# Performance work log

Measured on AMD Instinct MI355X. Metric: run time of the kernel, lower is better.

## Reference

```python
import jax, jax.numpy as jnp
import numpy as np

B, T, EMB, NDIM = 8, 2048, 1024, 1024


def setup_inputs() -> dict:
    key = jax.random.key(0)
    k1, k2, k3, k4 = jax.random.split(key, 4)
    X = jax.random.normal(k1, (B, T, EMB), dtype=jnp.float32)
    # Linear(emb, ndim, bias=False); stored as [emb, ndim] so projection is X @ W.
    scale = 1.0 / np.sqrt(EMB)
    Wq = jax.random.normal(k2, (EMB, NDIM), dtype=jnp.float32) * scale
    Wk = jax.random.normal(k3, (EMB, NDIM), dtype=jnp.float32) * scale
    Wv = jax.random.normal(k4, (EMB, NDIM), dtype=jnp.float32) * scale
    return {"X": X, "Wq": Wq, "Wk": Wk, "Wv": Wv}


def reference(X, Wq, Wk, Wv):
    ndim = Wq.shape[-1]
    T_ = X.shape[1]
    Q = X @ Wq  # [B,T,ndim]
    K = X @ Wk  # [B,T,ndim]
    V = X @ Wv  # [B,T,ndim]
    # scores[b,t,s] = Q[b,t] . K[b,s], scaled by ndim^-0.5
    scores = jnp.einsum("btd,bsd->bts", Q, K) * (ndim ** -0.5)
    mask = jnp.tril(jnp.ones((T_, T_), dtype=bool))  # causal lower-triangular
    scores = jnp.where(mask, scores, -jnp.inf)
    # NOTE: source uses F.softmax(..., dim=1) -> normalize over the QUERY axis
    # (columns of the [T,T] matrix), not the usual key axis. Replicated faithfully.
    probs = jax.nn.softmax(scores, axis=1)
    # dropout is identity in eval / p=0 deterministic baseline
    return probs @ V  # [B,T,ndim]
```

## Files before the change

kernel.cpp:

```cpp
#include <hip/hip_runtime.h>
#include <hip/hip_bf16.h>

#define B_   8
#define T_   2048
#define EMB_ 1024
#define ND_  1024
#define NTB2 8

typedef __attribute__((ext_vector_type(8))) short   bf8_t;
typedef __attribute__((ext_vector_type(4))) float   f32x4;

__device__ __forceinline__ unsigned short f2bf(float f) {
  union { float f; unsigned int u; } c; c.f = f;
  unsigned int u = c.u;
  unsigned int r = (u + 0x7FFFu + ((u >> 16) & 1u)) >> 16;
  return (unsigned short)r;
}

__device__ __forceinline__ float bf2f(unsigned short b) {
  union { unsigned int u; float f; } c; c.u = ((unsigned int)b) << 16;
  return c.f;
}

__device__ __forceinline__ void gload_lds16(const unsigned short* g, unsigned short* l) {
  __builtin_amdgcn_global_load_lds(
      (const __attribute__((address_space(1))) unsigned int*)g,
      (__attribute__((address_space(3))) unsigned int*)l,
      16, 0, 0);
}

#define SB0() __builtin_amdgcn_sched_barrier(0)
#define BAR() __builtin_amdgcn_s_barrier()

__device__ __forceinline__ void stage_half(const unsigned short* __restrict__ g, int lda,
                                           unsigned short* lhalf, int wave, int lane) {
  const int r3 = lane >> 3, c3 = lane & 7;
  const int colsw = ((c3 ^ r3) << 3);
#pragma unroll
  for (int j = 0; j < 2; ++j) {
    const int row = wave * 8 + r3 + 64 * j;
    gload_lds16(g + (size_t)row * lda + colsw, lhalf + wave * 512 + j * 4096);
  }
}

__device__ __forceinline__ bf8_t read_frag(const unsigned short* half, int r, int ks, int lane) {
  const int col = (((ks) << 5) + ((lane >> 4) << 3)) ^ ((r & 7) << 3);
  return *(const bf8_t*)(half + r * 64 + col);
}

__device__ __forceinline__ int swz_ep(int x) { return ((x >> 1) & 7) << 4; }

__global__ void __launch_bounds__(256) cvt_x_kernel(const float* __restrict__ in,
                                                    unsigned short* __restrict__ out) {
  const int i = (blockIdx.x * 256 + threadIdx.x) * 4;
  float4 v = *(const float4*)(in + i);
  ushort4 o = make_ushort4(f2bf(v.x), f2bf(v.y), f2bf(v.z), f2bf(v.w));
  *(ushort4*)(out + i) = o;
}

__global__ void __launch_bounds__(256) transpose_w3_kernel(const float* __restrict__ Wq,
                                                           const float* __restrict__ Wk,
                                                           const float* __restrict__ Wv,
                                                           unsigned short* __restrict__ Wt3) {
  __shared__ unsigned short tile[32][33];
  const int z = blockIdx.z;
  const float* W = (z == 0) ? Wq : (z == 1) ? Wk : Wv;
  const float cscale = (z == 0) ? 0.03125f : 1.0f;
  unsigned short* Wt = Wt3 + (size_t)z * ND_ * EMB_;
  const int n0 = blockIdx.x * 32, k0 = blockIdx.y * 32;
  const int tx = threadIdx.x & 31, ty = threadIdx.x >> 5;
#pragma unroll
  for (int r = 0; r < 32; r += 8) {
    float v = W[(size_t)(k0 + ty + r) * ND_ + n0 + tx];
    tile[tx][ty + r] = f2bf(v * cscale);
  }
  __syncthreads();
#pragma unroll
  for (int r = 0; r < 32; r += 8) {
    Wt[(size_t)(n0 + ty + r) * EMB_ + k0 + tx] = tile[ty + r][tx];
  }
}

#define MFMA_QUAD(MB, AF, AOFF) do { \
  __builtin_amdgcn_s_setprio(1); \
  _Pragma("unroll") \
  for (int mi = 0; mi < 2; ++mi) \
    _Pragma("unroll") \
    for (int nf = 0; nf < 4; ++nf) \
      _Pragma("unroll") \
      for (int ks = 0; ks < 2; ++ks) \
        acc[(MB) * 2 + mi][nf] = __builtin_amdgcn_mfma_f32_16x16x32_bf16( \
            (AF)[(AOFF) + mi][ks], bfr[nf][ks], acc[(MB) * 2 + mi][nf], 0, 0, 0); \
  __builtin_amdgcn_s_setprio(0); \
} while (0)

#define MFMA_Q8(MB) do { \
  __builtin_amdgcn_s_setprio(1); \
  _Pragma("unroll") \
  for (int nf = 0; nf < 4; ++nf) \
    _Pragma("unroll") \
    for (int ks = 0; ks < 2; ++ks) \
      acc[(MB)][nf] = __builtin_amdgcn_mfma_f32_16x16x32_bf16( \
          af[(MB)][ks], bfr[nf][ks], acc[(MB)][nf], 0, 0, 0); \
  __builtin_amdgcn_s_setprio(0); \
} while (0)

#define LDSA(d, h) (lds256 + ((d) * 2 + (h)) * 8192)
#define LDSB(d, h) (lds256 + 32768 + ((d) * 2 + (h)) * 8192)

#define GEMM256_LOOP(ABASE, BBASE, LDK) \
  stage_half((ABASE),                             (LDK), LDSA(0, 0), wave, lane); \
  stage_half((ABASE) + (size_t)128 * (LDK),       (LDK), LDSA(0, 1), wave, lane); \
  stage_half((BBASE),                             (LDK), LDSB(0, 0), wave, lane); \
  stage_half((BBASE) + (size_t)128 * (LDK),       (LDK), LDSB(0, 1), wave, lane); \
  stage_half((BBASE) + 64,                        (LDK), LDSB(1, 0), wave, lane); \
  stage_half((BBASE) + (size_t)128 * (LDK) + 64,  (LDK), LDSB(1, 1), wave, lane); \
  stage_half((ABASE) + 64,                        (LDK), LDSA(1, 0), wave, lane); \
  stage_half((ABASE) + (size_t)128 * (LDK) + 64,  (LDK), LDSA(1, 1), wave, lane); \
  asm volatile("s_waitcnt vmcnt(8)" ::: "memory"); \
  SB0(); BAR(); SB0(); \
  for (int t = 0; t < 16; ++t) { \
    const int d = t & 1; \
    const unsigned short* Ah = LDSA(d, wm); \
    const unsigned short* Bh = LDSB(d, wn >> 1); \
    bf8_t bfr[4][2], af[4][2]; \
    _Pragma("unroll") \
    for (int nf = 0; nf < 4; ++nf) \
      _Pragma("unroll") \
      for (int ks = 0; ks < 2; ++ks) bfr[nf][ks] = read_frag(Bh, brow + nf * 16, ks, lane); \
    _Pragma("unroll") \
    for (int mf = 0; mf < 4; ++mf) \
      _Pragma("unroll") \
      for (int ks = 0; ks < 2; ++ks) af[mf][ks] = read_frag(Ah, arow + mf * 16, ks, lane); \
    SB0(); BAR(); SB0(); \
    MFMA_QUAD(0, af, 0); \
    SB0(); \
    asm volatile("s_waitcnt lgkmcnt(0)" ::: "memory"); \
    SB0(); BAR(); SB0(); \
    if (t < 14) { \
      stage_half((BBASE) + (size_t)(t + 2) * 64,                     (LDK), LDSB(d, 0), wave, lane); \
      stage_half((BBASE) + (size_t)128 * (LDK) + (size_t)(t + 2) * 64,(LDK), LDSB(d, 1), wave, lane); \
    } \
    SB0(); BAR(); SB0(); \
    MFMA_QUAD(1, af, 2); \
    SB0(); BAR(); SB0(); \
    bf8_t af2[4][2]; \
    _Pragma("unroll") \
    for (int mf = 0; mf < 4; ++mf) \
      _Pragma("unroll") \
      for (int ks = 0; ks < 2; ++ks) af2[mf][ks] = read_frag(Ah, arow + (mf + 4) * 16, ks, lane); \
    SB0(); BAR(); SB0(); \
    MFMA_QUAD(2, af2, 0); \
    SB0(); \
    asm volatile("s_waitcnt lgkmcnt(0)" ::: "memory"); \
    SB0(); BAR(); SB0(); \
    if (t < 14) { \
      stage_half((ABASE) + (size_t)(t + 2) * 64,                     (LDK), LDSA(d, 0), wave, lane); \
      stage_half((ABASE) + (size_t)128 * (LDK) + (size_t)(t + 2) * 64,(LDK), LDSA(d, 1), wave, lane); \
      asm volatile("s_waitcnt vmcnt(8)" ::: "memory"); \
    } else if (t == 14) { \
      asm volatile("s_waitcnt vmcnt(0)" ::: "memory"); \
    } \
    SB0(); BAR(); SB0(); \
    MFMA_QUAD(3, af2, 2); \
    SB0(); BAR(); SB0(); \
  }

template <int OUTMODE>
__global__ void __launch_bounds__(512, 2)
gemm_xw256_kernel(const unsigned short* __restrict__ A,
                  const unsigned short* __restrict__ Bt,
                  unsigned short* __restrict__ C) {
  extern __shared__ unsigned short lds256[];
  const int tid = threadIdx.x, lane = tid & 63, wave = tid >> 6;
  const int wm = wave >> 2, wn = wave & 3;
  const int m0 = blockIdx.y * 256, n0 = blockIdx.x * 256;
  const unsigned short* Ab = A + (size_t)m0 * EMB_;
  const unsigned short* Bb = Bt + (size_t)n0 * EMB_;
  f32x4 acc[8][4];
#pragma unroll
  for (int i = 0; i < 8; ++i)
#pragma unroll
    for (int j = 0; j < 4; ++j)
#pragma unroll
      for (int q = 0; q < 4; ++q) acc[i][j][q] = 0.f;
  const int arow = lane & 15;
  const int brow = (wn & 1) * 64 + (lane & 15);

  GEMM256_LOOP(Ab, Bb, EMB_)

  const int cc = lane & 15, cr4 = (lane >> 4) << 2;
#pragma unroll
  for (int mf = 0; mf < 8; ++mf)
#pragma unroll
    for (int nf = 0; nf < 4; ++nf)
#pragma unroll
      for (int q = 0; q < 4; ++q) {
        const int r = wm * 128 + mf * 16 + cr4 + q;
        const int c = wn * 64 + nf * 16 + cc;
        const unsigned short bv = f2bf(acc[mf][nf][q]);
        const int byte = (OUTMODE == 1) ? (c * 512 + ((r * 2) ^ swz_ep(c)))
                                        : (r * 512 + ((c * 2) ^ swz_ep(r)));
        lds256[byte >> 1] = bv;
      }
  __syncthreads();
  if (OUTMODE == 0) {
#pragma unroll
    for (int p = 0; p < 16; ++p) {
      const int o = p * 8192 + tid * 16;
      const int ri = o >> 9, cb = o & 511;
      const bf8_t v = *(const bf8_t*)(lds256 + (((o & ~511) | (cb ^ swz_ep(ri))) >> 1));
      *(bf8_t*)(C + (size_t)(m0 + ri) * ND_ + n0 + (cb >> 1)) = v;
    }
  } else {
    const int bb = m0 >> 11, tt0 = m0 & 2047;
#pragma unroll
    for (int p = 0; p < 16; ++p) {
      const int o = p * 8192 + tid * 16;
      const int ci = o >> 9, rb = o & 511;
      const bf8_t v = *(const bf8_t*)(lds256 + (((o & ~511) | (rb ^ swz_ep(ci))) >> 1));
      *(bf8_t*)(C + ((size_t)bb * ND_ + n0 + ci) * T_ + tt0 + (rb >> 1)) = v;
    }
  }
}

__global__ void __launch_bounds__(512, 2)
scoretile576_kernel(const unsigned short* __restrict__ Qb,
                    const unsigned short* __restrict__ Kb,
                    unsigned short* __restrict__ Pp,
                    float* __restrict__ pm) {
  extern __shared__ unsigned short lds256[];
  const int id = blockIdx.x;
  const int b = id & 7;
  const int r = id >> 3;
  int sc = 0, pfx = 0;
#pragma unroll 8
  for (int i = 0; i < 8; ++i) {
    const int cnt = 16 - 2 * sc;
    if (pfx + cnt <= r) { pfx += cnt; ++sc; }
  }
  const int tr = 2 * sc + (r - pfx);
  const int t0 = tr * 128, s0 = sc * 256;
  const int tid = threadIdx.x, lane = tid & 63, wave = tid >> 6;
  const int wm = wave >> 2, wn = wave & 3;
  const int arow = lane & 15;
  const unsigned short* Ab = Qb + ((size_t)b * T_ + t0) * ND_;
  const unsigned short* Bb = Kb + ((size_t)b * T_ + s0) * ND_;
  f32x4 acc[4][4];
#pragma unroll
  for (int i = 0; i < 4; ++i)
#pragma unroll
    for (int j = 0; j < 4; ++j)
#pragma unroll
      for (int q = 0; q < 4; ++q) acc[i][j][q] = 0.f;

  stage_half(Ab,                           ND_, lds256,                     wave, lane);
  stage_half(Bb,                           ND_, lds256 + 16384,             wave, lane);
  stage_half(Bb + (size_t)128 * ND_,       ND_, lds256 + 16384 + 8192,      wave, lane);
  stage_half(Ab + 64,                      ND_, lds256 + 8192,              wave, lane);
  stage_half(Bb + 64,                      ND_, lds256 + 16384 + 2 * 8192,  wave, lane);
  stage_half(Bb + (size_t)128 * ND_ + 64,  ND_, lds256 + 16384 + 3 * 8192,  wave, lane);
  asm volatile("s_waitcnt vmcnt(6)" ::: "memory");
  SB0(); BAR(); SB0();

  for (int t = 0; t < 16; ++t) {
    const int d = t & 1;
    const unsigned short* Ah = lds256 + d * 8192;
    const unsigned short* Bh = lds256 + 16384 + (d * 2 + (wn >> 1)) * 8192;
    bf8_t bfr[4][2], af[4][2];
#pragma unroll
    for (int nf = 0; nf < 4; ++nf)
#pragma unroll
      for (int ks = 0; ks < 2; ++ks)
        bfr[nf][ks] = read_frag(Bh, (wn & 1) * 64 + nf * 16 + arow, ks, lane);
#pragma unroll
    for (int mf = 0; mf < 4; ++mf)
#pragma unroll
      for (int ks = 0; ks < 2; ++ks)
        af[mf][ks] = read_frag(Ah, wm * 64 + mf * 16 + arow, ks, lane);
    SB0(); BAR(); SB0();
    MFMA_Q8(0);
    SB0();
    asm volatile("s_waitcnt lgkmcnt(0)" ::: "memory");
    SB0(); BAR(); SB0();
    if (t < 14) {
      stage_half(Ab + (size_t)(t + 2) * 64, ND_, lds256 + d * 8192, wave, lane);
      stage_half(Bb + (size_t)(t + 2) * 64, ND_, lds256 + 16384 + (d * 2) * 8192, wave, lane);
    }
    SB0(); BAR(); SB0();
    MFMA_Q8(1);
    SB0(); BAR(); SB0();
    if (t < 14)
      stage_half(Bb + (size_t)128 * ND_ + (size_t)(t + 2) * 64, ND_, lds256 + 16384 + (d * 2 + 1) * 8192, wave, lane);
    SB0(); BAR(); SB0();
    MFMA_Q8(2);
    SB0(); BAR(); SB0();
    if (t < 14)      { asm volatile("s_waitcnt vmcnt(6)" ::: "memory"); }
    else if (t == 14){ asm volatile("s_waitcnt vmcnt(0)" ::: "memory"); }
    SB0(); BAR(); SB0();
    MFMA_Q8(3);
    SB0(); BAR(); SB0();
  }

  __syncthreads();
  const int cc = lane & 15, cr4 = (lane >> 4) << 2;
  float csum[4];
#pragma unroll
  for (int nf = 0; nf < 4; ++nf) csum[nf] = 0.f;
#pragma unroll
  for (int mf = 0; mf < 4; ++mf)
#pragma unroll
    for (int nf = 0; nf < 4; ++nf)
#pragma unroll
      for (int q = 0; q < 4; ++q) {
        const int rr = wm * 64 + mf * 16 + cr4 + q;
        const int c  = wn * 64 + nf * 16 + cc;
        const bool ok = (t0 + rr) >= (s0 + c);
        unsigned short bv = 0;
        if (ok) {
          bv = f2bf(__expf(fminf(acc[mf][nf][q], 30.f)));
          csum[nf] += bf2f(bv);
        }
        lds256[(rr * 512 + ((c * 2) ^ swz_ep(rr))) >> 1] = bv;
      }
  __syncthreads();
  unsigned short* Pbase = Pp + (size_t)b * T_ * T_;
#pragma unroll
  for (int p = 0; p < 8; ++p) {
    const int o = p * 8192 + tid * 16;
    const int ri = o >> 9, cb = o & 511;
    const bf8_t v = *(const bf8_t*)(lds256 + (((o & ~511) | (cb ^ swz_ep(ri))) >> 1));
    *(bf8_t*)(Pbase + (size_t)(t0 + ri) * T_ + s0 + (cb >> 1)) = v;
  }
#pragma unroll
  for (int nf = 0; nf < 4; ++nf) {
    csum[nf] += __shfl_xor(csum[nf], 16);
    csum[nf] += __shfl_xor(csum[nf], 32);
  }
  __syncthreads();
  float* red = (float*)lds256;
  if (lane < 16) {
#pragma unroll
    for (int nf = 0; nf < 4; ++nf)
      red[((wm * 4 + wn) * 4 + nf) * 16 + lane] = csum[nf];
  }
  __syncthreads();
  if (wm == 0 && lane < 16) {
    const size_t base = (((size_t)b * 8 + sc) * 16 + tr) * 256;
#pragma unroll
    for (int nf = 0; nf < 4; ++nf) {
      const float s = red[((0 * 4 + wn) * 4 + nf) * 16 + lane] +
                      red[((1 * 4 + wn) * 4 + nf) * 16 + lane];
      pm[base + wn * 64 + nf * 16 + lane] = s;
    }
  }
}

__global__ void __launch_bounds__(256) colreduce_kernel(const float* __restrict__ pm,
                                                        float* __restrict__ colinv) {
  const int sc = blockIdx.x, b = blockIdx.y, c = threadIdx.x;
  float l = 0.f;
  for (int tr = 2 * sc; tr < 16; ++tr)
    l += pm[(((size_t)b * 8 + sc) * 16 + tr) * 256 + c];
  colinv[(size_t)b * T_ + sc * 256 + c] = 1.0f / l;
}

__global__ void __launch_bounds__(256) vscale_kernel(unsigned short* __restrict__ Vt,
                                                     const float* __restrict__ colinv) {
  const int idx = blockIdx.x * 256 + threadIdx.x;
  const int s8 = (idx * 8) & (T_ - 1);
  const int bd = idx / (T_ / 8);
  const int b = bd >> 10;
  unsigned short* p = Vt + (size_t)bd * T_ + s8;
  bf8_t v = *(bf8_t*)p;
#pragma unroll
  for (int j = 0; j < 8; ++j) {
    const float f = bf2f((unsigned short)v[j]) * colinv[(size_t)b * T_ + s8 + j];
    v[j] = (short)f2bf(f);
  }
  *(bf8_t*)p = v;
}

__device__ __forceinline__ void pv_segment(const unsigned short* __restrict__ Ab,
                                           const unsigned short* __restrict__ Bb,
                                           float* __restrict__ Cb,
                                           int ktiles, unsigned short* lds256,
                                           int lane, int wave) {
  const int wm = wave >> 2, wn = wave & 3;
  const int arow = lane & 15;
  f32x4 acc[4][4];
#pragma unroll
  for (int i = 0; i < 4; ++i)
#pragma unroll
    for (int j = 0; j < 4; ++j)
#pragma unroll
      for (int q = 0; q < 4; ++q) acc[i][j][q] = 0.f;

  stage_half(Ab,                           T_, lds256,                     wave, lane);
  stage_half(Bb,                           T_, lds256 + 16384,             wave, lane);
  stage_half(Bb + (size_t)128 * T_,        T_, lds256 + 16384 + 8192,      wave, lane);
  stage_half(Ab + 64,                      T_, lds256 + 8192,              wave, lane);
  stage_half(Bb + 64,                      T_, lds256 + 16384 + 2 * 8192,  wave, lane);
  stage_half(Bb + (size_t)128 * T_ + 64,   T_, lds256 + 16384 + 3 * 8192,  wave, lane);
  asm volatile("s_waitcnt vmcnt(6)" ::: "memory");
  SB0(); BAR(); SB0();

  for (int t = 0; t < ktiles; ++t) {
    const int d = t & 1;
    const unsigned short* Ah = lds256 + d * 8192;
    const unsigned short* Bh = lds256 + 16384 + (d * 2 + (wn >> 1)) * 8192;
    bf8_t bfr[4][2], af[4][2];
#pragma unroll
    for (int nf = 0; nf < 4; ++nf)
#pragma unroll
      for (int ks = 0; ks < 2; ++ks)
        bfr[nf][ks] = read_frag(Bh, (wn & 1) * 64 + nf * 16 + arow, ks, lane);
#pragma unroll
    for (int mf = 0; mf < 4; ++mf)
#pragma unroll
      for (int ks = 0; ks < 2; ++ks)
        af[mf][ks] = read_frag(Ah, wm * 64 + mf * 16 + arow, ks, lane);
    SB0(); BAR(); SB0();
    MFMA_Q8(0);
    SB0();
    asm volatile("s_waitcnt lgkmcnt(0)" ::: "memory");
    SB0(); BAR(); SB0();
    if (t < ktiles - 2) {
      stage_half(Ab + (size_t)(t + 2) * 64, T_, lds256 + d * 8192, wave, lane);
      stage_half(Bb + (size_t)(t + 2) * 64, T_, lds256 + 16384 + (d * 2) * 8192, wave, lane);
    }
    SB0(); BAR(); SB0();
    MFMA_Q8(1);
    SB0(); BAR(); SB0();
    if (t < ktiles - 2)
      stage_half(Bb + (size_t)128 * T_ + (size_t)(t + 2) * 64, T_, lds256 + 16384 + (d * 2 + 1) * 8192, wave, lane);
    SB0(); BAR(); SB0();
    MFMA_Q8(2);
    SB0(); BAR(); SB0();
    if (t < ktiles - 2)      { asm volatile("s_waitcnt vmcnt(6)" ::: "memory"); }
    else if (t == ktiles - 2){ asm volatile("s_waitcnt vmcnt(0)" ::: "memory"); }
    SB0(); BAR(); SB0();
    MFMA_Q8(3);
    SB0(); BAR(); SB0();
  }

  const int cc = lane & 15, cr4 = (lane >> 4) << 2;
#pragma unroll
  for (int mf = 0; mf < 4; ++mf)
#pragma unroll
    for (int nf = 0; nf < 4; ++nf)
#pragma unroll
      for (int q = 0; q < 4; ++q) {
        const int row = wm * 64 + mf * 16 + cr4 + q;
        const int col = wn * 64 + nf * 16 + cc;
        Cb[(size_t)row * ND_ + col] = acc[mf][nf][q];
      }
}

__global__ void __launch_bounds__(512, 2)
gemm_pv512_kernel(const unsigned short* __restrict__ Pb,
                  const unsigned short* __restrict__ Vt,
                  float* __restrict__ out) {
  extern __shared__ unsigned short lds256[];
  const int id = blockIdx.x;
  const int tb = 15 - (id >> 5);
  const int ncol = (id >> 3) & 3;
  const int b = id & 7;
  const int lane = threadIdx.x & 63, wave = threadIdx.x >> 6;
  const int ktiles = 2 * tb + 2;
  pv_segment(Pb + (size_t)b * T_ * T_ + (size_t)tb * 128 * T_,
             Vt + (size_t)b * ND_ * T_ + (size_t)ncol * 256 * T_,
             out + (size_t)b * T_ * ND_ + (size_t)tb * 128 * ND_ + ncol * 256,
             ktiles, lds256, lane, wave);
}

extern "C" void kernel_launch(void* const* d_in, const int* in_sizes, int n_in,
                              void* d_out, int out_size, void* d_ws, size_t ws_size,
                              hipStream_t stream) {
  const float* X  = (const float*)d_in[0];
  const float* Wq = (const float*)d_in[1];
  const float* Wk = (const float*)d_in[2];
  const float* Wv = (const float*)d_in[3];
  float* out = (float*)d_out;
  (void)in_sizes; (void)n_in; (void)out_size;

  char* ws = (char*)d_ws;
  size_t off = 0;
  auto alloc = [&](size_t bytes) {
    void* p = ws + off;
    off += (bytes + 255) & ~(size_t)255;
    return p;
  };
  unsigned short* Xb  = (unsigned short*)alloc((size_t)B_ * T_ * EMB_ * 2);
  unsigned short* Wt3 = (unsigned short*)alloc((size_t)3 * ND_ * EMB_ * 2);
  unsigned short* Qb  = (unsigned short*)alloc((size_t)B_ * T_ * ND_ * 2);
  unsigned short* Kb  = (unsigned short*)alloc((size_t)B_ * T_ * ND_ * 2);
  unsigned short* Vt  = (unsigned short*)alloc((size_t)B_ * ND_ * T_ * 2);
  float* colinv = (float*)alloc((size_t)B_ * T_ * 4);
  float* pm     = (float*)alloc((size_t)B_ * 8 * 16 * 256 * 4);
  unsigned short* Pb  = (unsigned short*)alloc((size_t)B_ * T_ * T_ * 2);
  if (off > ws_size) return;

  hipFuncSetAttribute((const void*)&gemm_xw256_kernel<0>,
                      hipFuncAttributeMaxDynamicSharedMemorySize, 131072);
  hipFuncSetAttribute((const void*)&gemm_xw256_kernel<1>,
                      hipFuncAttributeMaxDynamicSharedMemorySize, 131072);
  hipFuncSetAttribute((const void*)&scoretile576_kernel,
                      hipFuncAttributeMaxDynamicSharedMemorySize, 98304);
  hipFuncSetAttribute((const void*)&gemm_pv512_kernel,
                      hipFuncAttributeMaxDynamicSharedMemorySize, 98304);

  hipLaunchKernelGGL(cvt_x_kernel, dim3((B_ * T_ * EMB_) / 1024), dim3(256), 0, stream, X, Xb);
  hipLaunchKernelGGL(transpose_w3_kernel, dim3(32, 32, 3), dim3(256), 0, stream, Wq, Wk, Wv, Wt3);
  hipLaunchKernelGGL((gemm_xw256_kernel<0>), dim3(ND_ / 256, (B_ * T_) / 256), dim3(512), 131072, stream,
                     Xb, Wt3, Qb);
  hipLaunchKernelGGL((gemm_xw256_kernel<0>), dim3(ND_ / 256, (B_ * T_) / 256), dim3(512), 131072, stream,
                     Xb, Wt3 + (size_t)ND_ * EMB_, Kb);
  hipLaunchKernelGGL((gemm_xw256_kernel<1>), dim3(ND_ / 256, (B_ * T_) / 256), dim3(512), 131072, stream,
                     Xb, Wt3 + (size_t)2 * ND_ * EMB_, Vt);
  hipLaunchKernelGGL(scoretile576_kernel, dim3(576), dim3(512), 98304, stream, Qb, Kb, Pb, pm);
  hipLaunchKernelGGL(colreduce_kernel, dim3(8, B_), dim3(256), 0, stream, pm, colinv);
  hipLaunchKernelGGL(vscale_kernel, dim3((B_ * ND_ * T_) / 8 / 256), dim3(256), 0, stream, Vt, colinv);
  hipLaunchKernelGGL(gemm_pv512_kernel, dim3(512), dim3(512), 98304, stream, Pb, Vt, out);
}
```

Before: 275.8 us.

## Single-buffer A tile in score and PV GEMMs to cut LDS footprint

The score and PV GEMM loops now share a macro that keeps one LDS buffer for the A tile while keeping B double-buffered. Dynamic LDS drops from 96KB to 80KB and launch bounds are raised to 4 blocks per CU. The goal is more resident blocks to hide latency. In exchange, A has only one-step prefetch and is overwritten mid-iteration, which shortens overlap and raises register pressure under the tighter launch bound. Whether LDS still allows 4 blocks per CU depends on the hardware's LDS capacity.

```diff
diff --git a/kernel.cpp b/kernel.cpp
--- a/kernel.cpp
+++ b/kernel.cpp
@@ -166,6 +166,52 @@
     SB0(); BAR(); SB0(); \
   }
 
+#define FB80(lds, d, h) ((lds) + 8192 + ((d) * 2 + (h)) * 8192)
+
+#define FLAT80_LOOP(LDSP, ABASE, BBASE, LDK, KT) \
+  stage_half((ABASE),                             (LDK), (LDSP),           wave, lane); \
+  stage_half((BBASE),                             (LDK), FB80(LDSP, 0, 0), wave, lane); \
+  stage_half((BBASE) + (size_t)128 * (LDK),       (LDK), FB80(LDSP, 0, 1), wave, lane); \
+  stage_half((BBASE) + 64,                        (LDK), FB80(LDSP, 1, 0), wave, lane); \
+  stage_half((BBASE) + (size_t)128 * (LDK) + 64,  (LDK), FB80(LDSP, 1, 1), wave, lane); \
+  asm volatile("s_waitcnt vmcnt(4)" ::: "memory"); \
+  SB0(); BAR(); SB0(); \
+  for (int t = 0; t < (KT); ++t) { \
+    const int d = t & 1; \
+    const unsigned short* Ah = (LDSP); \
+    const unsigned short* Bh = FB80(LDSP, d, wn >> 1); \
+    bf8_t bfr[4][2], af[4][2]; \
+    _Pragma("unroll") \
+    for (int nf = 0; nf < 4; ++nf) \
+      _Pragma("unroll") \
+      for (int ks = 0; ks < 2; ++ks) \
+        bfr[nf][ks] = read_frag(Bh, (wn & 1) * 64 + nf * 16 + arow, ks, lane); \
+    _Pragma("unroll") \
+    for (int mf = 0; mf < 4; ++mf) \
+      _Pragma("unroll") \
+      for (int ks = 0; ks < 2; ++ks) \
+        af[mf][ks] = read_frag(Ah, wm * 64 + mf * 16 + arow, ks, lane); \
+    SB0(); BAR(); SB0(); \
+    MFMA_Q8(0); \
+    SB0(); \
+    asm volatile("s_waitcnt lgkmcnt(0)" ::: "memory"); \
+    SB0(); BAR(); SB0(); \
+    if (t < (KT) - 1) stage_half((ABASE) + (size_t)(t + 1) * 64, (LDK), (LDSP), wave, lane); \
+    if (t < (KT) - 2) stage_half((BBASE) + (size_t)(t + 2) * 64, (LDK), FB80(LDSP, d, 0), wave, lane); \
+    SB0(); BAR(); SB0(); \
+    MFMA_Q8(1); \
+    SB0(); BAR(); SB0(); \
+    if (t < (KT) - 2) stage_half((BBASE) + (size_t)128 * (LDK) + (size_t)(t + 2) * 64, (LDK), FB80(LDSP, d, 1), wave, lane); \
+    SB0(); BAR(); SB0(); \
+    MFMA_Q8(2); \
+    SB0(); BAR(); SB0(); \
+    if (t < (KT) - 2)      { asm volatile("s_waitcnt vmcnt(4)" ::: "memory"); } \
+    else if (t == (KT) - 2){ asm volatile("s_waitcnt vmcnt(0)" ::: "memory"); } \
+    SB0(); BAR(); SB0(); \
+    MFMA_Q8(3); \
+    SB0(); BAR(); SB0(); \
+  }
+
 template <int OUTMODE>
 __global__ void __launch_bounds__(512, 2)
 gemm_xw256_kernel(const unsigned short* __restrict__ A,
@@ -224,7 +270,7 @@
   }
 }
 
-__global__ void __launch_bounds__(512, 2)
+__global__ void __launch_bounds__(512, 4)
 scoretile576_kernel(const unsigned short* __restrict__ Qb,
                     const unsigned short* __restrict__ Kb,
                     unsigned short* __restrict__ Pp,
@@ -254,53 +300,7 @@
 #pragma unroll
       for (int q = 0; q < 4; ++q) acc[i][j][q] = 0.f;
 
-  stage_half(Ab,                           ND_, lds256,                     wave, lane);
-  stage_half(Bb,                           ND_, lds256 + 16384,             wave, lane);
-  stage_half(Bb + (size_t)128 * ND_,       ND_, lds256 + 16384 + 8192,      wave, lane);
-  stage_half(Ab + 64,                      ND_, lds256 + 8192,              wave, lane);
-  stage_half(Bb + 64,                      ND_, lds256 + 16384 + 2 * 8192,  wave, lane);
-  stage_half(Bb + (size_t)128 * ND_ + 64,  ND_, lds256 + 16384 + 3 * 8192,  wave, lane);
-  asm volatile("s_waitcnt vmcnt(6)" ::: "memory");
-  SB0(); BAR(); SB0();
-
-  for (int t = 0; t < 16; ++t) {
-    const int d = t & 1;
-    const unsigned short* Ah = lds256 + d * 8192;
-    const unsigned short* Bh = lds256 + 16384 + (d * 2 + (wn >> 1)) * 8192;
-    bf8_t bfr[4][2], af[4][2];
-#pragma unroll
-    for (int nf = 0; nf < 4; ++nf)
-#pragma unroll
-      for (int ks = 0; ks < 2; ++ks)
-        bfr[nf][ks] = read_frag(Bh, (wn & 1) * 64 + nf * 16 + arow, ks, lane);
-#pragma unroll
-    for (int mf = 0; mf < 4; ++mf)
-#pragma unroll
-      for (int ks = 0; ks < 2; ++ks)
-        af[mf][ks] = read_frag(Ah, wm * 64 + mf * 16 + arow, ks, lane);
-    SB0(); BAR(); SB0();
-    MFMA_Q8(0);
-    SB0();
-    asm volatile("s_waitcnt lgkmcnt(0)" ::: "memory");
-    SB0(); BAR(); SB0();
-    if (t < 14) {
-      stage_half(Ab + (size_t)(t + 2) * 64, ND_, lds256 + d * 8192, wave, lane);
-      stage_half(Bb + (size_t)(t + 2) * 64, ND_, lds256 + 16384 + (d * 2) * 8192, wave, lane);
-    }
-    SB0(); BAR(); SB0();
-    MFMA_Q8(1);
-    SB0(); BAR(); SB0();
-    if (t < 14)
-      stage_half(Bb + (size_t)128 * ND_ + (size_t)(t + 2) * 64, ND_, lds256 + 16384 + (d * 2 + 1) * 8192, wave, lane);
-    SB0(); BAR(); SB0();
-    MFMA_Q8(2);
-    SB0(); BAR(); SB0();
-    if (t < 14)      { asm volatile("s_waitcnt vmcnt(6)" ::: "memory"); }
-    else if (t == 14){ asm volatile("s_waitcnt vmcnt(0)" ::: "memory"); }
-    SB0(); BAR(); SB0();
-    MFMA_Q8(3);
-    SB0(); BAR(); SB0();
-  }
+  FLAT80_LOOP(lds256, Ab, Bb, ND_, 16)
 
   __syncthreads();
   const int cc = lane & 15, cr4 = (lane >> 4) << 2;
@@ -381,83 +381,7 @@
   *(bf8_t*)p = v;
 }
 
-__device__ __forceinline__ void pv_segment(const unsigned short* __restrict__ Ab,
-                                           const unsigned short* __restrict__ Bb,
-                                           float* __restrict__ Cb,
-                                           int ktiles, unsigned short* lds256,
-                                           int lane, int wave) {
-  const int wm = wave >> 2, wn = wave & 3;
-  const int arow = lane & 15;
-  f32x4 acc[4][4];
-#pragma unroll
-  for (int i = 0; i < 4; ++i)
-#pragma unroll
-    for (int j = 0; j < 4; ++j)
-#pragma unroll
-      for (int q = 0; q < 4; ++q) acc[i][j][q] = 0.f;
-
-  stage_half(Ab,                           T_, lds256,                     wave, lane);
-  stage_half(Bb,                           T_, lds256 + 16384,             wave, lane);
-  stage_half(Bb + (size_t)128 * T_,        T_, lds256 + 16384 + 8192,      wave, lane);
-  stage_half(Ab + 64,                      T_, lds256 + 8192,              wave, lane);
-  stage_half(Bb + 64,                      T_, lds256 + 16384 + 2 * 8192,  wave, lane);
-  stage_half(Bb + (size_t)128 * T_ + 64,   T_, lds256 + 16384 + 3 * 8192,  wave, lane);
-  asm volatile("s_waitcnt vmcnt(6)" ::: "memory");
-  SB0(); BAR(); SB0();
-
-  for (int t = 0; t < ktiles; ++t) {
-    const int d = t & 1;
-    const unsigned short* Ah = lds256 + d * 8192;
-    const unsigned short* Bh = lds256 + 16384 + (d * 2 + (wn >> 1)) * 8192;
-    bf8_t bfr[4][2], af[4][2];
-#pragma unroll
-    for (int nf = 0; nf < 4; ++nf)
-#pragma unroll
-      for (int ks = 0; ks < 2; ++ks)
-        bfr[nf][ks] = read_frag(Bh, (wn & 1) * 64 + nf * 16 + arow, ks, lane);
-#pragma unroll
-    for (int mf = 0; mf < 4; ++mf)
-#pragma unroll
-      for (int ks = 0; ks < 2; ++ks)
-        af[mf][ks] = read_frag(Ah, wm * 64 + mf * 16 + arow, ks, lane);
-    SB0(); BAR(); SB0();
-    MFMA_Q8(0);
-    SB0();
-    asm volatile("s_waitcnt lgkmcnt(0)" ::: "memory");
-    SB0(); BAR(); SB0();
-    if (t < ktiles - 2) {
-      stage_half(Ab + (size_t)(t + 2) * 64, T_, lds256 + d * 8192, wave, lane);
-      stage_half(Bb + (size_t)(t + 2) * 64, T_, lds256 + 16384 + (d * 2) * 8192, wave, lane);
-    }
-    SB0(); BAR(); SB0();
-    MFMA_Q8(1);
-    SB0(); BAR(); SB0();
-    if (t < ktiles - 2)
-      stage_half(Bb + (size_t)128 * T_ + (size_t)(t + 2) * 64, T_, lds256 + 16384 + (d * 2 + 1) * 8192, wave, lane);
-    SB0(); BAR(); SB0();
-    MFMA_Q8(2);
-    SB0(); BAR(); SB0();
-    if (t < ktiles - 2)      { asm volatile("s_waitcnt vmcnt(6)" ::: "memory"); }
-    else if (t == ktiles - 2){ asm volatile("s_waitcnt vmcnt(0)" ::: "memory"); }
-    SB0(); BAR(); SB0();
-    MFMA_Q8(3);
-    SB0(); BAR(); SB0();
-  }
-
-  const int cc = lane & 15, cr4 = (lane >> 4) << 2;
-#pragma unroll
-  for (int mf = 0; mf < 4; ++mf)
-#pragma unroll
-    for (int nf = 0; nf < 4; ++nf)
-#pragma unroll
-      for (int q = 0; q < 4; ++q) {
-        const int row = wm * 64 + mf * 16 + cr4 + q;
-        const int col = wn * 64 + nf * 16 + cc;
-        Cb[(size_t)row * ND_ + col] = acc[mf][nf][q];
-      }
-}
-
-__global__ void __launch_bounds__(512, 2)
+__global__ void __launch_bounds__(512, 4)
 gemm_pv512_kernel(const unsigned short* __restrict__ Pb,
                   const unsigned short* __restrict__ Vt,
                   float* __restrict__ out) {
@@ -467,11 +391,34 @@
   const int ncol = (id >> 3) & 3;
   const int b = id & 7;
   const int lane = threadIdx.x & 63, wave = threadIdx.x >> 6;
+  const int wm = wave >> 2, wn = wave & 3;
+  const int arow = lane & 15;
   const int ktiles = 2 * tb + 2;
-  pv_segment(Pb + (size_t)b * T_ * T_ + (size_t)tb * 128 * T_,
-             Vt + (size_t)b * ND_ * T_ + (size_t)ncol * 256 * T_,
-             out + (size_t)b * T_ * ND_ + (size_t)tb * 128 * ND_ + ncol * 256,
-             ktiles, lds256, lane, wave);
+  const unsigned short* Ab = Pb + (size_t)b * T_ * T_ + (size_t)tb * 128 * T_;
+  const unsigned short* Bb = Vt + (size_t)b * ND_ * T_ + (size_t)ncol * 256 * T_;
+  float* Cb = out + (size_t)b * T_ * ND_ + (size_t)tb * 128 * ND_ + ncol * 256;
+
+  f32x4 acc[4][4];
+#pragma unroll
+  for (int i = 0; i < 4; ++i)
+#pragma unroll
+    for (int j = 0; j < 4; ++j)
+#pragma unroll
+      for (int q = 0; q < 4; ++q) acc[i][j][q] = 0.f;
+
+  FLAT80_LOOP(lds256, Ab, Bb, T_, ktiles)
+
+  const int cc = lane & 15, cr4 = (lane >> 4) << 2;
+#pragma unroll
+  for (int mf = 0; mf < 4; ++mf)
+#pragma unroll
+    for (int nf = 0; nf < 4; ++nf)
+#pragma unroll
+      for (int q = 0; q < 4; ++q) {
+        const int row = wm * 64 + mf * 16 + cr4 + q;
+        const int col = wn * 64 + nf * 16 + cc;
+        Cb[(size_t)row * ND_ + col] = acc[mf][nf][q];
+      }
 }
 
 extern "C" void kernel_launch(void* const* d_in, const int* in_sizes, int n_in,
@@ -506,9 +453,9 @@
   hipFuncSetAttribute((const void*)&gemm_xw256_kernel<1>,
                       hipFuncAttributeMaxDynamicSharedMemorySize, 131072);
   hipFuncSetAttribute((const void*)&scoretile576_kernel,
-                      hipFuncAttributeMaxDynamicSharedMemorySize, 98304);
+                      hipFuncAttributeMaxDynamicSharedMemorySize, 81920);
   hipFuncSetAttribute((const void*)&gemm_pv512_kernel,
-                      hipFuncAttributeMaxDynamicSharedMemorySize, 98304);
+                      hipFuncAttributeMaxDynamicSharedMemorySize, 81920);
 
   hipLaunchKernelGGL(cvt_x_kernel, dim3((B_ * T_ * EMB_) / 1024), dim3(256), 0, stream, X, Xb);
   hipLaunchKernelGGL(transpose_w3_kernel, dim3(32, 32, 3), dim3(256), 0, stream, Wq, Wk, Wv, Wt3);
@@ -518,8 +465,8 @@
                      Xb, Wt3 + (size_t)ND_ * EMB_, Kb);
   hipLaunchKernelGGL((gemm_xw256_kernel<1>), dim3(ND_ / 256, (B_ * T_) / 256), dim3(512), 131072, stream,
                      Xb, Wt3 + (size_t)2 * ND_ * EMB_, Vt);
-  hipLaunchKernelGGL(scoretile576_kernel, dim3(576), dim3(512), 98304, stream, Qb, Kb, Pb, pm);
+  hipLaunchKernelGGL(scoretile576_kernel, dim3(576), dim3(512), 81920, stream, Qb, Kb, Pb, pm);
   hipLaunchKernelGGL(colreduce_kernel, dim3(8, B_), dim3(256), 0, stream, pm, colinv);
   hipLaunchKernelGGL(vscale_kernel, dim3((B_ * ND_ * T_) / 8 / 256), dim3(256), 0, stream, Vt, colinv);
-  hipLaunchKernelGGL(gemm_pv512_kernel, dim3(512), dim3(512), 98304, stream, Pb, Vt, out);
-}
+  hipLaunchKernelGGL(gemm_pv512_kernel, dim3(512), dim3(512), 81920, stream, Pb, Vt, out);
+}
```

After: 415.2 us. 1.51x slower.
